# Performance work log

Measured on AMD Instinct MI355X. Metric: run time of the kernel, lower is better.

The kernel has to match this reference:

```python
import jax, jax.numpy as jnp
import numpy as np

NUM_NODE = 65536      # destination nodes in this layer
NUM_SRC = 262144      # rows of x (sampled source nodes)
DEG = 16              # uniform degree -> num_edge = NUM_NODE*DEG
NUM_EDGE = NUM_NODE * DEG
IN_CH = 128
HID_CH = 128
NUM_REL = 8


def setup_inputs() -> dict:
    key = jax.random.key(0)
    ks = jax.random.split(key, 8)
    x = jax.random.normal(ks[0], (NUM_SRC, IN_CH), dtype=jnp.float32)
    # glorot-style init for relation weights [R, in, hid]
    scale = jnp.sqrt(6.0 / (IN_CH + HID_CH))
    weight = jax.random.uniform(ks[1], (NUM_REL, IN_CH, HID_CH), dtype=jnp.float32,
                                minval=-scale, maxval=scale)
    history_buffer = jax.random.normal(ks[2], (NUM_NODE, HID_CH), dtype=jnp.float32)
    ptr = jnp.arange(NUM_NODE + 1, dtype=jnp.int64) * DEG  # uniform-degree CSR
    idx = jax.random.randint(ks[3], (NUM_EDGE,), 0, NUM_SRC, dtype=jnp.int64)
    edge_types = jax.random.randint(ks[4], (NUM_EDGE,), 0, NUM_REL, dtype=jnp.int64)
    used_mask = jax.random.uniform(ks[5], (NUM_SRC,)) < 0.95
    # history_map: -1 means no cached entry; >=0 means overwrite from buffer
    history_map = jax.random.randint(ks[6], (NUM_NODE,), -1, 5, dtype=jnp.int64)
    return {
        "x": x, "weight": weight, "history_buffer": history_buffer,
        "ptr": ptr, "idx": idx, "edge_types": edge_types,
        "used_mask": used_mask, "history_map": history_map,
        "history_size": HID_CH, "num_node": NUM_NODE,
    }


def reference(x, weight, history_buffer, ptr, idx, edge_types, used_mask,
              history_map, history_size, num_node):
    num_rel = weight.shape[0]
    num_edge = idx.shape[0]          # == ptr[num_node] by construction
    hid = weight.shape[2]
    fdt = x.dtype

    deg = ptr[1:num_node + 1] - ptr[:num_node]                 # [N]
    dst = jnp.repeat(jnp.arange(num_node), deg,
                     total_repeat_length=num_edge)             # [E]
    src = idx                                                  # [E]
    # edges whose source is not "used" get relation num_rel -> no weight group
    rel = jnp.where(used_mask[src], edge_types, num_rel)       # [E]

    # relation-grouped GEMM + gather, expressed as masked accumulation
    # (avoids materializing [E, in, hid] gathered weights)
    msg = jnp.zeros((num_edge, hid), dtype=fdt)
    for r in range(num_rel):
        h_r = x @ weight[r]                                    # [Nsrc, hid]
        msg = msg + jnp.where((rel == r)[:, None], h_r[src], jnp.zeros((), fdt))

    out = jax.ops.segment_sum(msg, dst, num_segments=num_node) # scatter-add
    out = out / deg.astype(fdt)[:, None]                       # degree norm

    if history_size > 0:
        cached = (history_map != -1)[:, None]
        out = jnp.where(cached, history_buffer, out)           # history overwrite
    # original returns (out, his) with his aliasing out
    return out
```

## Files before the change

### kernel.cpp

```cpp
#include <hip/hip_runtime.h>
#include <hip/hip_bf16.h>
#include <stdint.h>

typedef __attribute__((ext_vector_type(4))) float f32x4;
typedef __attribute__((ext_vector_type(8))) short bf16x8;

#define NCH  128
#define NREL 8
#define NSEG 32
#define SEGCAP 2048

__device__ __forceinline__ unsigned short f2bf(float f) {
    unsigned u = __builtin_bit_cast(unsigned, f);
    u += 0x7fffu + ((u >> 16) & 1u);
    return (unsigned short)(u >> 16);
}

__device__ __forceinline__ bool mask_used(const unsigned char* um, int stride, int s) {
    if (stride == 1) return um[s] != 0;
    if (stride == 4) return ((const int*)um)[s] != 0;
    return ((const long long*)um)[s] != 0;
}

__global__ __launch_bounds__(256)
void k_prep(const float* __restrict__ W, unsigned short* __restrict__ Wb,
            int* __restrict__ cn, const unsigned char* __restrict__ um_raw) {
    int o = blockIdx.x * 256 + threadIdx.x;
    if (o < NREL * NCH * NCH) {
        int kk = o & 31;
        int h  = (o >> 5) & (NCH - 1);
        int kt = o >> 12;
        Wb[o] = f2bf(W[(kt * 32 + kk) * NCH + h]);
    }
    if (blockIdx.x == 0) {
        __shared__ unsigned sA, sB;
        const int t = threadIdx.x;
        if (t == 0) { sA = 0; sB = 0; }
        if (t < NSEG) cn[16 + t * 16] = 0;
        __syncthreads();
        unsigned a = 0, b = 0;
        #pragma unroll 4
        for (int p = t; p < 1024; p += 256) {
            unsigned v = um_raw[p];
            if ((p & 3) != 0) a |= v;
            if ((p & 7) == 4) b |= v;
        }
        if (a) atomicOr(&sA, 1u);
        if (b) atomicOr(&sB, 1u);
        __syncthreads();
        if (t == 0) cn[1] = sA ? 1 : (sB ? 4 : 8);
    }
}

__global__ __launch_bounds__(256)
void k_hist(const float* __restrict__ hb, const int* __restrict__ hm,
            const int* __restrict__ hs, float* __restrict__ out,
            int* __restrict__ cn, int* __restrict__ glist, int num_node) {
    __shared__ int cList[32], ncList[32];
    __shared__ int nCs, nNCs, gbase;
    const int t = threadIdx.x;
    if (t < 64) {
        const int n = blockIdx.x * 32 + t;
        const bool valid  = (t < 32) && (n < num_node);
        const bool cached = valid && (hs[0] > 0) && (hm[n] != -1);
        const bool nc     = valid && !cached;
        const unsigned long long mC  = __ballot(cached);
        const unsigned long long mNC = __ballot(nc);
        const unsigned long long below = (1ull << t) - 1;
        if (cached) cList[__popcll(mC & below)]   = n;
        if (nc)     ncList[__popcll(mNC & below)] = n;
        if (t == 0) { nCs = __popcll(mC); nNCs = __popcll(mNC); }
    }
    __syncthreads();
    const int myC = nCs, myNC = nNCs;
    const int hw = t >> 5, l = t & 31;
    int   node[4];
    f32x4 v[4];
    #pragma unroll 4
    for (int j = 0; j < 4; ++j) {
        const int i = hw + j * 8;
        node[j] = (i < myC) ? cList[i] : -1;
        if (node[j] >= 0)
            v[j] = *(const f32x4*)(hb + (long)node[j] * NCH + l * 4);
    }
    #pragma unroll 4
    for (int j = 0; j < 4; ++j) {
        if (node[j] >= 0)
            __builtin_nontemporal_store(v[j],
                (f32x4*)(out + (long)node[j] * NCH + l * 4));
    }
    const int seg = blockIdx.x & (NSEG - 1);
    if (t == 0) gbase = atomicAdd(&cn[16 + seg * 16], myNC);
    __syncthreads();
    if (t < myNC) glist[seg * SEGCAP + gbase + t] = ncList[t];
}

__global__ __launch_bounds__(512, 4)
void k_main(const float* __restrict__ x, const unsigned short* __restrict__ Wb,
            const int* __restrict__ ptr, const int* __restrict__ idx,
            const int* __restrict__ et, const unsigned char* __restrict__ um,
            const int* __restrict__ cn, const int* __restrict__ glist,
            float* __restrict__ out) {
    __shared__ __align__(16) char As[16 * NREL * NCH * 2];
    __shared__ int   nid[16];
    __shared__ float invdeg[16];

    const int seg   = blockIdx.x & (NSEG - 1);
    const int grp   = blockIdx.x >> 5;
    const int cntS  = cn[16 + seg * 16];
    const int base  = grp * 16;
    if (base >= cntS) return;
    const int mstride = cn[1];
    const int t = threadIdx.x;
    if (t < 16) {
        const int i = base + t;
        nid[t]    = (i < cntS) ? glist[seg * SEGCAP + i] : -1;
        invdeg[t] = 0.0f;
    }
    __syncthreads();

    const int hw    = t >> 5;
    const int l     = t & 31;
    const int lbase = t & 32;
    const int n     = nid[hw];

    if (n >= 0) {
        const int p0 = ptr[n], p1 = ptr[n + 1];
        const int deg = p1 - p0;
        if (l == 0) invdeg[hw] = (deg > 0) ? 1.0f / (float)deg : 0.0f;
        int myPk = NREL << 24;
        if (l < 16 && (p0 + l) < p1) {
            const int e  = p0 + l;
            const int s  = idx[e];
            const int tt = et[e];
            myPk = s | (((mask_used(um, mstride, s) && tt >= 0 && tt < NREL)
                         ? tt : NREL) << 24);
        }
        int   pk[16];
        f32x4 xv[16];
        #pragma unroll 16
        for (int e = 0; e < 16; ++e) {
            pk[e] = __shfl(myPk, lbase + e, 64);
            xv[e] = *(const f32x4*)(x + (long)(pk[e] & 0xFFFFFF) * NCH + l * 4);
        }
        float acc[NREL][4];
        #pragma unroll
        for (int q = 0; q < NREL; ++q)
            #pragma unroll
            for (int j = 0; j < 4; ++j) acc[q][j] = 0.0f;
        #pragma unroll 16
        for (int e = 0; e < 16; ++e) {
            const int r = pk[e] >> 24;
            #pragma unroll
            for (int q = 0; q < NREL; ++q) {
                const float sel = (r == q) ? 1.0f : 0.0f;
                acc[q][0] += sel * xv[e].x;
                acc[q][1] += sel * xv[e].y;
                acc[q][2] += sel * xv[e].z;
                acc[q][3] += sel * xv[e].w;
            }
        }
        for (int e = p0 + 16; e < p1; ++e) {
            const int s  = idx[e];
            const int tt = et[e];
            if (mask_used(um, mstride, s) && tt >= 0 && tt < NREL) {
                const f32x4 w = *(const f32x4*)(x + (long)s * NCH + l * 4);
                #pragma unroll
                for (int q = 0; q < NREL; ++q) {
                    const float sel = (tt == q) ? 1.0f : 0.0f;
                    acc[q][0] += sel * w.x;
                    acc[q][1] += sel * w.y;
                    acc[q][2] += sel * w.z;
                    acc[q][3] += sel * w.w;
                }
            }
        }
        #pragma unroll
        for (int q = 0; q < NREL; ++q) {
            ushort4 pkv;
            pkv.x = f2bf(acc[q][0]); pkv.y = f2bf(acc[q][1]);
            pkv.z = f2bf(acc[q][2]); pkv.w = f2bf(acc[q][3]);
            const int eb   = (q * NCH + l * 4) * 2;
            const int addr = (hw * 2048 + eb) ^ ((hw & 7) << 4);
            *(ushort4*)(As + addr) = pkv;
        }
    }
    __syncthreads();

    const int wv   = t >> 6;
    const int lane = t & 63;
    const int row  = lane & 15;
    const int koff = (lane >> 4) * 8;
    const int col0 = wv * 16 + row;
    f32x4 c0 = {0.f, 0.f, 0.f, 0.f};
    #pragma unroll 8
    for (int kt = 0; kt < 32; ++kt) {
        const int aaddr = (row * 2048 + (kt * 32 + koff) * 2) ^ ((row & 7) << 4);
        const bf16x8 a  = *(const bf16x8*)(As + aaddr);
        const bf16x8 b0 = *(const bf16x8*)(Wb + ((kt * NCH + col0) << 5) + koff);
        c0 = __builtin_amdgcn_mfma_f32_16x16x32_bf16(a, b0, c0, 0, 0, 0);
    }

    __syncthreads();
    float* Cs = (float*)As;
    {
        const int r4 = (lane >> 4) * 4;
        #pragma unroll
        for (int j = 0; j < 4; ++j) {
            const int rr = r4 + j;
            Cs[rr * NCH + col0] = c0[j] * invdeg[rr];
        }
    }
    __syncthreads();
    {
        const int nn = nid[hw];
        if (nn >= 0) {
            const f32x4 vv = *(const f32x4*)(Cs + hw * NCH + l * 4);
            __builtin_nontemporal_store(vv,
                (f32x4*)(out + (long)nn * NCH + l * 4));
        }
    }
}

extern "C" void kernel_launch(void* const* d_in, const int* in_sizes, int n_in,
                              void* d_out, int out_size, void* d_ws, size_t ws_size,
                              hipStream_t stream) {
    const float*         x   = (const float*)d_in[0];
    const float*         W   = (const float*)d_in[1];
    const float*         hb  = (const float*)d_in[2];
    const int*           ptr = (const int*)d_in[3];
    const int*           idx = (const int*)d_in[4];
    const int*           et  = (const int*)d_in[5];
    const unsigned char* um  = (const unsigned char*)d_in[6];
    const int*           hm  = (const int*)d_in[7];
    const int*           hs  = (const int*)d_in[8];
    float* out = (float*)d_out;

    const int num_node = in_sizes[7];

    size_t off = 2560;
    int* cn    = (int*)d_ws;
    int* glist = (int*)((char*)d_ws + off);       off += (size_t)NSEG * SEGCAP * 4;
    unsigned short* Wb = (unsigned short*)((char*)d_ws + off);

    k_prep<<<(NREL * NCH * NCH + 255) / 256, 256, 0, stream>>>(W, Wb, cn, um);
    k_hist<<<(num_node + 31) / 32, 256, 0, stream>>>(hb, hm, hs, out, cn, glist, num_node);
    k_main<<<(num_node + 15) / 16, 512, 0, stream>>>(x, Wb, ptr, idx, et, um, cn, glist, out);
}
```

Measured before the change: 50.93 us.

## Fuse history copy into main kernel and build node list in prep

Drops the separate history kernel. Building the uncached-node list now happens in the prep kernel through per-wave ballots and atomics. Copying history-buffer rows for cached nodes moves into extra trailing blocks of the main kernel, so those copies can overlap the GEMM/gather work. The counters are zeroed with a memset, which adds a call but removes one launch. Launch bounds drop from 4 to 2 blocks per CU, which loosens register limits but may lower occupancy. The prep grid is also fixed at 512 blocks, which assumes num_node is at most 65536.

New measurement: 44.60 us (median of 2 runs). 1.14x faster.

```diff
diff --git a/kernel.cpp b/kernel.cpp
--- a/kernel.cpp
+++ b/kernel.cpp
@@ -24,86 +24,95 @@
 
 __global__ __launch_bounds__(256)
 void k_prep(const float* __restrict__ W, unsigned short* __restrict__ Wb,
-            int* __restrict__ cn, const unsigned char* __restrict__ um_raw) {
-    int o = blockIdx.x * 256 + threadIdx.x;
+            int* __restrict__ cn, const unsigned char* __restrict__ um_raw,
+            const int* __restrict__ hm, const int* __restrict__ hs,
+            int* __restrict__ glist, int num_node) {
+    const int t = threadIdx.x;
+    const int b = blockIdx.x;
+    const int o = b * 256 + t;
     if (o < NREL * NCH * NCH) {
-        int kk = o & 31;
-        int h  = (o >> 5) & (NCH - 1);
-        int kt = o >> 12;
-        Wb[o] = f2bf(W[(kt * 32 + kk) * NCH + h]);
-    }
-    if (blockIdx.x == 0) {
+        const int kk  = o & 31;
+        const int col = (o >> 5) & (NCH - 1);
+        const int kt  = o >> 12;
+        Wb[o] = f2bf(W[(kt * 32 + kk) * NCH + col]);
+    }
+    if (b < 256) {
+        const int w = t >> 6, l = t & 63;
+        const int n = b * 256 + w * 64 + l;
+        bool nc = false;
+        if (n < num_node) nc = !((hs[0] > 0) && (hm[n] != -1));
+        const unsigned long long m = __ballot(nc);
+        const int cnt = __popcll(m);
+        const int seg = (b * 4 + w) & (NSEG - 1);
+        int base = 0;
+        if (l == 0 && cnt) base = atomicAdd(&cn[16 + seg * 16], cnt);
+        base = __shfl(base, 0, 64);
+        if (nc)
+            glist[seg * SEGCAP + base + __popcll(m & ((1ull << l) - 1))] = n;
+    }
+    if (b == 0) {
         __shared__ unsigned sA, sB;
-        const int t = threadIdx.x;
         if (t == 0) { sA = 0; sB = 0; }
-        if (t < NSEG) cn[16 + t * 16] = 0;
         __syncthreads();
-        unsigned a = 0, b = 0;
+        unsigned a = 0, bb = 0;
         #pragma unroll 4
         for (int p = t; p < 1024; p += 256) {
-            unsigned v = um_raw[p];
+            const unsigned v = um_raw[p];
             if ((p & 3) != 0) a |= v;
-            if ((p & 7) == 4) b |= v;
-        }
-        if (a) atomicOr(&sA, 1u);
-        if (b) atomicOr(&sB, 1u);
+            if ((p & 7) == 4) bb |= v;
+        }
+        if (a)  atomicOr(&sA, 1u);
+        if (bb) atomicOr(&sB, 1u);
         __syncthreads();
         if (t == 0) cn[1] = sA ? 1 : (sB ? 4 : 8);
     }
 }
 
-__global__ __launch_bounds__(256)
-void k_hist(const float* __restrict__ hb, const int* __restrict__ hm,
-            const int* __restrict__ hs, float* __restrict__ out,
-            int* __restrict__ cn, int* __restrict__ glist, int num_node) {
-    __shared__ int cList[32], ncList[32];
-    __shared__ int nCs, nNCs, gbase;
-    const int t = threadIdx.x;
-    if (t < 64) {
-        const int n = blockIdx.x * 32 + t;
-        const bool valid  = (t < 32) && (n < num_node);
-        const bool cached = valid && (hs[0] > 0) && (hm[n] != -1);
-        const bool nc     = valid && !cached;
-        const unsigned long long mC  = __ballot(cached);
-        const unsigned long long mNC = __ballot(nc);
-        const unsigned long long below = (1ull << t) - 1;
-        if (cached) cList[__popcll(mC & below)]   = n;
-        if (nc)     ncList[__popcll(mNC & below)] = n;
-        if (t == 0) { nCs = __popcll(mC); nNCs = __popcll(mNC); }
-    }
-    __syncthreads();
-    const int myC = nCs, myNC = nNCs;
-    const int hw = t >> 5, l = t & 31;
-    int   node[4];
-    f32x4 v[4];
-    #pragma unroll 4
-    for (int j = 0; j < 4; ++j) {
-        const int i = hw + j * 8;
-        node[j] = (i < myC) ? cList[i] : -1;
-        if (node[j] >= 0)
-            v[j] = *(const f32x4*)(hb + (long)node[j] * NCH + l * 4);
-    }
-    #pragma unroll 4
-    for (int j = 0; j < 4; ++j) {
-        if (node[j] >= 0)
-            __builtin_nontemporal_store(v[j],
-                (f32x4*)(out + (long)node[j] * NCH + l * 4));
-    }
-    const int seg = blockIdx.x & (NSEG - 1);
-    if (t == 0) gbase = atomicAdd(&cn[16 + seg * 16], myNC);
-    __syncthreads();
-    if (t < myNC) glist[seg * SEGCAP + gbase + t] = ncList[t];
-}
-
-__global__ __launch_bounds__(512, 4)
-void k_main(const float* __restrict__ x, const unsigned short* __restrict__ Wb,
-            const int* __restrict__ ptr, const int* __restrict__ idx,
-            const int* __restrict__ et, const unsigned char* __restrict__ um,
-            const int* __restrict__ cn, const int* __restrict__ glist,
-            float* __restrict__ out) {
+__global__ __launch_bounds__(512, 2)
+void k_fused(const float* __restrict__ x, const unsigned short* __restrict__ Wb,
+             const int* __restrict__ ptr, const int* __restrict__ idx,
+             const int* __restrict__ et, const unsigned char* __restrict__ um,
+             const int* __restrict__ cn, const int* __restrict__ glist,
+             const float* __restrict__ hb, const int* __restrict__ hm,
+             const int* __restrict__ hs, float* __restrict__ out,
+             int num_node, int mainSlots) {
     __shared__ __align__(16) char As[16 * NREL * NCH * 2];
     __shared__ int   nid[16];
     __shared__ float invdeg[16];
+    __shared__ int   cList[64];
+    __shared__ int   nC_s;
+
+    const int t = threadIdx.x;
+
+    if ((int)blockIdx.x >= mainSlots) {
+        const int win = blockIdx.x - mainSlots;
+        if (t < 64) {
+            const int n = win * 64 + t;
+            const bool cached = (n < num_node) && (hs[0] > 0) && (hm[n] != -1);
+            const unsigned long long m = __ballot(cached);
+            if (cached) cList[__popcll(m & ((1ull << t) - 1))] = n;
+            if (t == 0) nC_s = __popcll(m);
+        }
+        __syncthreads();
+        const int nC = nC_s;
+        const int hw = t >> 5, l = t & 31;
+        int   node[4];
+        f32x4 v[4];
+        #pragma unroll 4
+        for (int j = 0; j < 4; ++j) {
+            const int i = hw + j * 16;
+            node[j] = (i < nC) ? cList[i] : -1;
+            if (node[j] >= 0)
+                v[j] = *(const f32x4*)(hb + (long)node[j] * NCH + l * 4);
+        }
+        #pragma unroll 4
+        for (int j = 0; j < 4; ++j) {
+            if (node[j] >= 0)
+                __builtin_nontemporal_store(v[j],
+                    (f32x4*)(out + (long)node[j] * NCH + l * 4));
+        }
+        return;
+    }
 
     const int seg   = blockIdx.x & (NSEG - 1);
     const int grp   = blockIdx.x >> 5;
@@ -111,7 +120,6 @@
     const int base  = grp * 16;
     if (base >= cntS) return;
     const int mstride = cn[1];
-    const int t = threadIdx.x;
     if (t < 16) {
         const int i = base + t;
         nid[t]    = (i < cntS) ? glist[seg * SEGCAP + i] : -1;
@@ -243,7 +251,11 @@
     int* glist = (int*)((char*)d_ws + off);       off += (size_t)NSEG * SEGCAP * 4;
     unsigned short* Wb = (unsigned short*)((char*)d_ws + off);
 
-    k_prep<<<(NREL * NCH * NCH + 255) / 256, 256, 0, stream>>>(W, Wb, cn, um);
-    k_hist<<<(num_node + 31) / 32, 256, 0, stream>>>(hb, hm, hs, out, cn, glist, num_node);
-    k_main<<<(num_node + 15) / 16, 512, 0, stream>>>(x, Wb, ptr, idx, et, um, cn, glist, out);
-}
+    const int mainSlots  = (num_node + 15) / 16;
+    const int copyBlocks = (num_node + 63) / 64;
+
+    hipMemsetAsync(cn, 0, 2560, stream);
+    k_prep<<<512, 256, 0, stream>>>(W, Wb, cn, um, hm, hs, glist, num_node);
+    k_fused<<<mainSlots + copyBlocks, 512, 0, stream>>>(
+        x, Wb, ptr, idx, et, um, cn, glist, hb, hm, hs, out, num_node, mainSlots);
+}
```

## Fuse history overwrite and compaction into main aggregation kernel

Applied to the files above, without the earlier changes.

Merges the history-copy/compaction kernel with the main gather+MFMA kernel. Each 512-thread block now takes 64 nodes, copies the cached rows, and loops over groups of 16 non-cached nodes. This removes the global segmented list, its atomics and one kernel launch. In exchange each block runs a serial loop of up to four groups with extra barriers, and occupancy drops to 2 blocks per SIMD, which may reduce latency hiding for the irregular gathers.

New measurement: 79.86 us. 56.8% more time.

```diff
diff --git a/kernel.cpp b/kernel.cpp
--- a/kernel.cpp
+++ b/kernel.cpp
@@ -7,8 +7,6 @@
 
 #define NCH  128
 #define NREL 8
-#define NSEG 32
-#define SEGCAP 2048
 
 __device__ __forceinline__ unsigned short f2bf(float f) {
     unsigned u = __builtin_bit_cast(unsigned, f);
@@ -25,23 +23,22 @@
 __global__ __launch_bounds__(256)
 void k_prep(const float* __restrict__ W, unsigned short* __restrict__ Wb,
             int* __restrict__ cn, const unsigned char* __restrict__ um_raw) {
-    int o = blockIdx.x * 256 + threadIdx.x;
-    if (o < NREL * NCH * NCH) {
-        int kk = o & 31;
-        int h  = (o >> 5) & (NCH - 1);
-        int kt = o >> 12;
-        Wb[o] = f2bf(W[(kt * 32 + kk) * NCH + h]);
+    const int t = threadIdx.x;
+    const int o = blockIdx.x * 256 + t;
+    {
+        const int kk  = o & 31;
+        const int col = (o >> 5) & (NCH - 1);
+        const int kt  = o >> 12;
+        Wb[o] = f2bf(W[(kt * 32 + kk) * NCH + col]);
     }
     if (blockIdx.x == 0) {
         __shared__ unsigned sA, sB;
-        const int t = threadIdx.x;
         if (t == 0) { sA = 0; sB = 0; }
-        if (t < NSEG) cn[16 + t * 16] = 0;
         __syncthreads();
         unsigned a = 0, b = 0;
         #pragma unroll 4
         for (int p = t; p < 1024; p += 256) {
-            unsigned v = um_raw[p];
+            const unsigned v = um_raw[p];
             if ((p & 3) != 0) a |= v;
             if ((p & 7) == 4) b |= v;
         }
@@ -52,16 +49,25 @@
     }
 }
 
-__global__ __launch_bounds__(256)
-void k_hist(const float* __restrict__ hb, const int* __restrict__ hm,
-            const int* __restrict__ hs, float* __restrict__ out,
-            int* __restrict__ cn, int* __restrict__ glist, int num_node) {
-    __shared__ int cList[32], ncList[32];
-    __shared__ int nCs, nNCs, gbase;
-    const int t = threadIdx.x;
+__global__ __launch_bounds__(512, 2)
+void k_fused(const float* __restrict__ x, const unsigned short* __restrict__ Wb,
+             const int* __restrict__ ptr, const int* __restrict__ idx,
+             const int* __restrict__ et, const unsigned char* __restrict__ um,
+             const int* __restrict__ cn, const float* __restrict__ hb,
+             const int* __restrict__ hm, const int* __restrict__ hs,
+             float* __restrict__ out, int num_node) {
+    __shared__ __align__(16) char As[16 * NREL * NCH * 2];
+    __shared__ int   cList[64], ncList[64];
+    __shared__ int   nC_s, nNC_s;
+    __shared__ int   nidg[16];
+    __shared__ float invdeg[16];
+
+    const int t  = threadIdx.x;
+    const int n0 = blockIdx.x * 64;
+
     if (t < 64) {
-        const int n = blockIdx.x * 32 + t;
-        const bool valid  = (t < 32) && (n < num_node);
+        const int n = n0 + t;
+        const bool valid  = n < num_node;
         const bool cached = valid && (hs[0] > 0) && (hm[n] != -1);
         const bool nc     = valid && !cached;
         const unsigned long long mC  = __ballot(cached);
@@ -69,156 +75,141 @@
         const unsigned long long below = (1ull << t) - 1;
         if (cached) cList[__popcll(mC & below)]   = n;
         if (nc)     ncList[__popcll(mNC & below)] = n;
-        if (t == 0) { nCs = __popcll(mC); nNCs = __popcll(mNC); }
+        if (t == 0) { nC_s = __popcll(mC); nNC_s = __popcll(mNC); }
     }
     __syncthreads();
-    const int myC = nCs, myNC = nNCs;
-    const int hw = t >> 5, l = t & 31;
-    int   node[4];
-    f32x4 v[4];
-    #pragma unroll 4
-    for (int j = 0; j < 4; ++j) {
-        const int i = hw + j * 8;
-        node[j] = (i < myC) ? cList[i] : -1;
-        if (node[j] >= 0)
-            v[j] = *(const f32x4*)(hb + (long)node[j] * NCH + l * 4);
-    }
-    #pragma unroll 4
-    for (int j = 0; j < 4; ++j) {
-        if (node[j] >= 0)
-            __builtin_nontemporal_store(v[j],
-                (f32x4*)(out + (long)node[j] * NCH + l * 4));
-    }
-    const int seg = blockIdx.x & (NSEG - 1);
-    if (t == 0) gbase = atomicAdd(&cn[16 + seg * 16], myNC);
-    __syncthreads();
-    if (t < myNC) glist[seg * SEGCAP + gbase + t] = ncList[t];
-}
-
-__global__ __launch_bounds__(512, 4)
-void k_main(const float* __restrict__ x, const unsigned short* __restrict__ Wb,
-            const int* __restrict__ ptr, const int* __restrict__ idx,
-            const int* __restrict__ et, const unsigned char* __restrict__ um,
-            const int* __restrict__ cn, const int* __restrict__ glist,
-            float* __restrict__ out) {
-    __shared__ __align__(16) char As[16 * NREL * NCH * 2];
-    __shared__ int   nid[16];
-    __shared__ float invdeg[16];
-
-    const int seg   = blockIdx.x & (NSEG - 1);
-    const int grp   = blockIdx.x >> 5;
-    const int cntS  = cn[16 + seg * 16];
-    const int base  = grp * 16;
-    if (base >= cntS) return;
-    const int mstride = cn[1];
-    const int t = threadIdx.x;
-    if (t < 16) {
-        const int i = base + t;
-        nid[t]    = (i < cntS) ? glist[seg * SEGCAP + i] : -1;
-        invdeg[t] = 0.0f;
-    }
-    __syncthreads();
-
+    const int nC  = nC_s;
+    const int nNC = nNC_s;
     const int hw    = t >> 5;
     const int l     = t & 31;
     const int lbase = t & 32;
-    const int n     = nid[hw];
-
-    if (n >= 0) {
-        const int p0 = ptr[n], p1 = ptr[n + 1];
-        const int deg = p1 - p0;
-        if (l == 0) invdeg[hw] = (deg > 0) ? 1.0f / (float)deg : 0.0f;
-        int myPk = NREL << 24;
-        if (l < 16 && (p0 + l) < p1) {
-            const int e  = p0 + l;
-            const int s  = idx[e];
-            const int tt = et[e];
-            myPk = s | (((mask_used(um, mstride, s) && tt >= 0 && tt < NREL)
-                         ? tt : NREL) << 24);
-        }
-        int   pk[16];
-        f32x4 xv[16];
-        #pragma unroll 16
-        for (int e = 0; e < 16; ++e) {
-            pk[e] = __shfl(myPk, lbase + e, 64);
-            xv[e] = *(const f32x4*)(x + (long)(pk[e] & 0xFFFFFF) * NCH + l * 4);
-        }
-        float acc[NREL][4];
-        #pragma unroll
-        for (int q = 0; q < NREL; ++q)
+    const int mstride = cn[1];
+
+    {
+        int   node[4];
+        f32x4 v[4];
+        #pragma unroll 4
+        for (int j = 0; j < 4; ++j) {
+            const int i = hw + j * 16;
+            node[j] = (i < nC) ? cList[i] : -1;
+            if (node[j] >= 0)
+                v[j] = *(const f32x4*)(hb + (long)node[j] * NCH + l * 4);
+        }
+        #pragma unroll 4
+        for (int j = 0; j < 4; ++j) {
+            if (node[j] >= 0)
+                __builtin_nontemporal_store(v[j],
+                    (f32x4*)(out + (long)node[j] * NCH + l * 4));
+        }
+    }
+
+    const int nGroups = (nNC + 15) >> 4;
+    for (int g = 0; g < nGroups; ++g) {
+        if (t < 16) {
+            const int i = g * 16 + t;
+            nidg[t]   = (i < nNC) ? ncList[i] : -1;
+            invdeg[t] = 0.0f;
+        }
+        __syncthreads();
+
+        const int n = nidg[hw];
+        if (n >= 0) {
+            const int p0 = ptr[n], p1 = ptr[n + 1];
+            const int deg = p1 - p0;
+            if (l == 0) invdeg[hw] = (deg > 0) ? 1.0f / (float)deg : 0.0f;
+            int myPk = NREL << 24;
+            if (l < 16 && (p0 + l) < p1) {
+                const int e  = p0 + l;
+                const int s  = idx[e];
+                const int tt = et[e];
+                myPk = s | (((mask_used(um, mstride, s) && tt >= 0 && tt < NREL)
+                             ? tt : NREL) << 24);
+            }
+            int   pk[16];
+            f32x4 xv[16];
+            #pragma unroll 16
+            for (int e = 0; e < 16; ++e) {
+                pk[e] = __shfl(myPk, lbase + e, 64);
+                xv[e] = *(const f32x4*)(x + (long)(pk[e] & 0xFFFFFF) * NCH + l * 4);
+            }
+            float acc[NREL][4];
             #pragma unroll
-            for (int j = 0; j < 4; ++j) acc[q][j] = 0.0f;
-        #pragma unroll 16
-        for (int e = 0; e < 16; ++e) {
-            const int r = pk[e] >> 24;
+            for (int q = 0; q < NREL; ++q)
+                #pragma unroll
+                for (int j = 0; j < 4; ++j) acc[q][j] = 0.0f;
+            #pragma unroll 16
+            for (int e = 0; e < 16; ++e) {
+                const int r = pk[e] >> 24;
+                #pragma unroll
+                for (int q = 0; q < NREL; ++q) {
+                    const float sel = (r == q) ? 1.0f : 0.0f;
+                    acc[q][0] += sel * xv[e].x;
+                    acc[q][1] += sel * xv[e].y;
+                    acc[q][2] += sel * xv[e].z;
+                    acc[q][3] += sel * xv[e].w;
+                }
+            }
+            for (int e = p0 + 16; e < p1; ++e) {
+                const int s  = idx[e];
+                const int tt = et[e];
+                if (mask_used(um, mstride, s) && tt >= 0 && tt < NREL) {
+                    const f32x4 w = *(const f32x4*)(x + (long)s * NCH + l * 4);
+                    #pragma unroll
+                    for (int q = 0; q < NREL; ++q) {
+                        const float sel = (tt == q) ? 1.0f : 0.0f;
+                        acc[q][0] += sel * w.x;
+                        acc[q][1] += sel * w.y;
+                        acc[q][2] += sel * w.z;
+                        acc[q][3] += sel * w.w;
+                    }
+                }
+            }
             #pragma unroll
             for (int q = 0; q < NREL; ++q) {
-                const float sel = (r == q) ? 1.0f : 0.0f;
-                acc[q][0] += sel * xv[e].x;
-                acc[q][1] += sel * xv[e].y;
-                acc[q][2] += sel * xv[e].z;
-                acc[q][3] += sel * xv[e].w;
-            }
-        }
-        for (int e = p0 + 16; e < p1; ++e) {
-            const int s  = idx[e];
-            const int tt = et[e];
-            if (mask_used(um, mstride, s) && tt >= 0 && tt < NREL) {
-                const f32x4 w = *(const f32x4*)(x + (long)s * NCH + l * 4);
-                #pragma unroll
-                for (int q = 0; q < NREL; ++q) {
-                    const float sel = (tt == q) ? 1.0f : 0.0f;
-                    acc[q][0] += sel * w.x;
-                    acc[q][1] += sel * w.y;
-                    acc[q][2] += sel * w.z;
-                    acc[q][3] += sel * w.w;
-                }
-            }
-        }
-        #pragma unroll
-        for (int q = 0; q < NREL; ++q) {
-            ushort4 pkv;
-            pkv.x = f2bf(acc[q][0]); pkv.y = f2bf(acc[q][1]);
-            pkv.z = f2bf(acc[q][2]); pkv.w = f2bf(acc[q][3]);
-            const int eb   = (q * NCH + l * 4) * 2;
-            const int addr = (hw * 2048 + eb) ^ ((hw & 7) << 4);
-            *(ushort4*)(As + addr) = pkv;
-        }
-    }
-    __syncthreads();
-
-    const int wv   = t >> 6;
-    const int lane = t & 63;
-    const int row  = lane & 15;
-    const int koff = (lane >> 4) * 8;
-    const int col0 = wv * 16 + row;
-    f32x4 c0 = {0.f, 0.f, 0.f, 0.f};
-    #pragma unroll 8
-    for (int kt = 0; kt < 32; ++kt) {
-        const int aaddr = (row * 2048 + (kt * 32 + koff) * 2) ^ ((row & 7) << 4);
-        const bf16x8 a  = *(const bf16x8*)(As + aaddr);
-        const bf16x8 b0 = *(const bf16x8*)(Wb + ((kt * NCH + col0) << 5) + koff);
-        c0 = __builtin_amdgcn_mfma_f32_16x16x32_bf16(a, b0, c0, 0, 0, 0);
-    }
-
-    __syncthreads();
-    float* Cs = (float*)As;
-    {
-        const int r4 = (lane >> 4) * 4;
-        #pragma unroll
-        for (int j = 0; j < 4; ++j) {
-            const int rr = r4 + j;
-            Cs[rr * NCH + col0] = c0[j] * invdeg[rr];
-        }
-    }
-    __syncthreads();
-    {
-        const int nn = nid[hw];
-        if (nn >= 0) {
-            const f32x4 vv = *(const f32x4*)(Cs + hw * NCH + l * 4);
-            __builtin_nontemporal_store(vv,
-                (f32x4*)(out + (long)nn * NCH + l * 4));
-        }
+                ushort4 pkv;
+                pkv.x = f2bf(acc[q][0]); pkv.y = f2bf(acc[q][1]);
+                pkv.z = f2bf(acc[q][2]); pkv.w = f2bf(acc[q][3]);
+                const int eb   = (q * NCH + l * 4) * 2;
+                const int addr = (hw * 2048 + eb) ^ ((hw & 7) << 4);
+                *(ushort4*)(As + addr) = pkv;
+            }
+        }
+        __syncthreads();
+
+        const int wv   = t >> 6;
+        const int lane = t & 63;
+        const int row  = lane & 15;
+        const int koff = (lane >> 4) * 8;
+        const int col0 = wv * 16 + row;
+        f32x4 c0 = {0.f, 0.f, 0.f, 0.f};
+        #pragma unroll 8
+        for (int kt = 0; kt < 32; ++kt) {
+            const int aaddr = (row * 2048 + (kt * 32 + koff) * 2) ^ ((row & 7) << 4);
+            const bf16x8 a  = *(const bf16x8*)(As + aaddr);
+            const bf16x8 b0 = *(const bf16x8*)(Wb + ((kt * NCH + col0) << 5) + koff);
+            c0 = __builtin_amdgcn_mfma_f32_16x16x32_bf16(a, b0, c0, 0, 0, 0);
+        }
+
+        __syncthreads();
+        float* Cs = (float*)As;
+        {
+            const int r4 = (lane >> 4) * 4;
+            #pragma unroll
+            for (int j = 0; j < 4; ++j) {
+                const int rr = r4 + j;
+                Cs[rr * NCH + col0] = c0[j] * invdeg[rr];
+            }
+        }
+        __syncthreads();
+        {
+            const int nn = nidg[hw];
+            if (nn >= 0) {
+                const f32x4 vv = *(const f32x4*)(Cs + hw * NCH + l * 4);
+                __builtin_nontemporal_store(vv,
+                    (f32x4*)(out + (long)nn * NCH + l * 4));
+            }
+        }
+        __syncthreads();
     }
 }
 
@@ -238,12 +229,10 @@
 
     const int num_node = in_sizes[7];
 
-    size_t off = 2560;
-    int* cn    = (int*)d_ws;
-    int* glist = (int*)((char*)d_ws + off);       off += (size_t)NSEG * SEGCAP * 4;
-    unsigned short* Wb = (unsigned short*)((char*)d_ws + off);
-
-    k_prep<<<(NREL * NCH * NCH + 255) / 256, 256, 0, stream>>>(W, Wb, cn, um);
-    k_hist<<<(num_node + 31) / 32, 256, 0, stream>>>(hb, hm, hs, out, cn, glist, num_node);
-    k_main<<<(num_node + 15) / 16, 512, 0, stream>>>(x, Wb, ptr, idx, et, um, cn, glist, out);
-}
+    int* cn = (int*)d_ws;
+    unsigned short* Wb = (unsigned short*)((char*)d_ws + 256);
+
+    k_prep<<<512, 256, 0, stream>>>(W, Wb, cn, um);
+    k_fused<<<(num_node + 63) / 64, 512, 0, stream>>>(
+        x, Wb, ptr, idx, et, um, cn, hb, hm, hs, out, num_node);
+}
```
